# Performance work log

Measured on AMD Instinct MI355X. Metric: run time of the kernel, lower is better.

## Reference

```python
import jax, jax.numpy as jnp
import numpy as np

B, S, D_IN, D_OUT = 4, 2048, 1024, 1024

def setup_inputs() -> dict:
    key = jax.random.key(0)
    kx, kq, kk, kv = jax.random.split(key, 4)
    x = jax.random.normal(kx, (B, S, D_IN), dtype=jnp.float32)
    # nn.Linear weights are [d_out, d_in]; init scale ~ 1/sqrt(d_in)
    sc = 1.0 / np.sqrt(D_IN)
    Wq = jax.random.uniform(kq, (D_OUT, D_IN), minval=-sc, maxval=sc, dtype=jnp.float32)
    Wk = jax.random.uniform(kk, (D_OUT, D_IN), minval=-sc, maxval=sc, dtype=jnp.float32)
    Wv = jax.random.uniform(kv, (D_OUT, D_IN), minval=-sc, maxval=sc, dtype=jnp.float32)
    return {"x": x, "Wq": Wq, "Wk": Wk, "Wv": Wv}

def reference(x, Wq, Wk, Wv):
    # QKV projections (Linear without bias): y = x @ W.T
    q = jnp.einsum('bsd,od->bso', x, Wq)
    k = jnp.einsum('bsd,od->bso', x, Wk)
    v = jnp.einsum('bsd,od->bso', x, Wv)
    scores = jnp.einsum('bqo,bko->bqk', q, k)
    # NOTE: original code calls masked_fill non-in-place and discards the
    # result, so no causal mask is actually applied. Faithful: no mask.
    scale = 1.0 / jnp.sqrt(jnp.asarray(k.shape[-1], dtype=scores.dtype))
    weights = jax.nn.softmax(scores * scale, axis=-1)
    # dropout p=0.0 -> identity
    return jnp.einsum('bqk,bko->bqo', weights, v)
```

## Files before the change

### kernel.cpp

```cpp
#include <hip/hip_runtime.h>
#include <hip/hip_bf16.h>
#include <stdint.h>


typedef short bf16x8 __attribute__((ext_vector_type(8)));
typedef float f32x4  __attribute__((ext_vector_type(4)));

__device__ __forceinline__ unsigned short f2bf(float f) {
  unsigned u = __float_as_uint(f);
  u += 0x7fff + ((u >> 16) & 1);
  return (unsigned short)(u >> 16);
}

__global__ __launch_bounds__(256) void cvt_bf16(const float* __restrict__ src,
                                                unsigned short* __restrict__ dst) {
  int i = (blockIdx.x * 256 + threadIdx.x) * 4;
  float4 v = *(const float4*)(src + i);
  ushort4 o;
  o.x = f2bf(v.x); o.y = f2bf(v.y); o.z = f2bf(v.z); o.w = f2bf(v.w);
  *(ushort4*)(dst + i) = o;
}

__global__ __launch_bounds__(256) void invert8k(float* __restrict__ p) {
  int i = blockIdx.x * 256 + threadIdx.x;
  p[i] = 1.0f / p[i];
}

__device__ __forceinline__ void gload_lds16(const void* g, void* l) {
  __builtin_amdgcn_global_load_lds(
      (const __attribute__((address_space(1))) unsigned int*)g,
      (__attribute__((address_space(3))) unsigned int*)l, 16, 0, 0);
}

template<int STORE>
__global__ __launch_bounds__(256, 2) void gemm_nt(
    const unsigned short* __restrict__ A, const unsigned short* __restrict__ B,
    void* __restrict__ Cv, float* __restrict__ aux, int lda, int ldb, int ldc, int K,
    long strideA, long strideB, long strideC) {
  __shared__ __align__(16) unsigned short lds[2][2][128 * 32];
  const int tid  = threadIdx.x;
  const int lane = tid & 63;
  const int wid  = tid >> 6;
  const int bz   = blockIdx.z;
  const unsigned short* Ab = A + (size_t)bz * strideA;
  const unsigned short* Bb = B + (size_t)bz * strideB;
  const int row0 = blockIdx.x * 128;
  const int col0 = blockIdx.y * 128;

  f32x4 acc[4][4];
#pragma unroll
  for (int m = 0; m < 4; ++m)
#pragma unroll
    for (int n = 0; n < 4; ++n) acc[m][n] = f32x4{0.f, 0.f, 0.f, 0.f};

  const int KT = K >> 5;

  auto stage = [&](int buf, int kt) {
    const int k0 = kt << 5;
#pragma unroll
    for (int it = 0; it < 2; ++it) {
      int j   = it * 256 + tid;
      int r   = j >> 2;
      int kg  = j & 3;
      int kgS = kg ^ ((r >> 1) & 3);
      gload_lds16(Ab + (size_t)(row0 + r) * lda + k0 + kgS * 8, &lds[buf][0][j * 8]);
      gload_lds16(Bb + (size_t)(col0 + r) * ldb + k0 + kgS * 8, &lds[buf][1][j * 8]);
    }
  };

  stage(0, 0);
  int buf = 0;
  for (int kt = 0; kt < KT; ++kt) {
    __syncthreads();
    if (kt + 1 < KT) stage(buf ^ 1, kt + 1);
    const unsigned short* As = &lds[buf][0][0];
    const unsigned short* Bs = &lds[buf][1][0];
    const int kg = lane >> 4;
    const int lr = lane & 15;
    bf16x8 af[4], bfr[4];
#pragma unroll
    for (int m = 0; m < 4; ++m) {
      int r = ((wid >> 1) * 64) + m * 16 + lr;
      af[m] = *(const bf16x8*)(As + r * 32 + ((kg ^ ((r >> 1) & 3)) * 8));
    }
#pragma unroll
    for (int n = 0; n < 4; ++n) {
      int c = ((wid & 1) * 64) + n * 16 + lr;
      bfr[n] = *(const bf16x8*)(Bs + c * 32 + ((kg ^ ((c >> 1) & 3)) * 8));
    }
#pragma unroll
    for (int m = 0; m < 4; ++m)
#pragma unroll
      for (int n = 0; n < 4; ++n)
        acc[m][n] = __builtin_amdgcn_mfma_f32_16x16x32_bf16(af[m], bfr[n], acc[m][n], 0, 0, 0);
    buf ^= 1;
  }

  const int wr0 = row0 + (wid >> 1) * 64;
  const int wc0 = col0 + (wid & 1) * 64;
  const int rj  = lane >> 4;
  const int cl  = lane & 15;
  if constexpr (STORE == 3) {
    unsigned short* E = (unsigned short*)Cv + (size_t)bz * 4194304;
    float* rs = aux + bz * 2048;
    const float SC = 0.045084220027780106f;
#pragma unroll
    for (int m = 0; m < 4; ++m) {
#pragma unroll
      for (int j = 0; j < 4; ++j) {
        int r = wr0 + m * 16 + rj * 4 + j;
        float part = 0.f;
#pragma unroll
        for (int n = 0; n < 4; ++n) {
          int c = wc0 + n * 16 + cl;
          unsigned short eb = f2bf(exp2f(acc[m][n][j] * SC));
          E[(size_t)r * 2048 + c] = eb;
          part += __uint_as_float((unsigned)eb << 16);
        }
#pragma unroll
        for (int o = 1; o < 16; o <<= 1) part += __shfl_xor(part, o);
        if (cl == 0) atomicAdd(&rs[r], part);
      }
    }
  } else {
#pragma unroll
    for (int m = 0; m < 4; ++m) {
#pragma unroll
      for (int n = 0; n < 4; ++n) {
#pragma unroll
        for (int j = 0; j < 4; ++j) {
          int r = wr0 + m * 16 + rj * 4 + j;
          int c = wc0 + n * 16 + cl;
          float val = acc[m][n][j];
          if constexpr (STORE == 0) {
            unsigned short* C = (unsigned short*)Cv + (size_t)bz * strideC;
            C[(size_t)r * ldc + c] = f2bf(val);
          } else if constexpr (STORE == 2) {
            unsigned short* C = (unsigned short*)Cv;
            size_t idx = ((size_t)(r >> 11) * 1024 + c) * 2048 + (size_t)(r & 2047);
            C[idx] = f2bf(val);
          } else {
            float* C = (float*)Cv + (size_t)bz * strideC;
            C[(size_t)r * ldc + c] = val * aux[bz * 2048 + r];
          }
        }
      }
    }
  }
}

extern "C" void kernel_launch(void* const* d_in, const int* in_sizes, int n_in,
                              void* d_out, int out_size, void* d_ws, size_t ws_size,
                              hipStream_t stream) {
  const float* x  = (const float*)d_in[0];
  const float* Wq = (const float*)d_in[1];
  const float* Wk = (const float*)d_in[2];
  const float* Wv = (const float*)d_in[3];

  char* w = (char*)d_ws;
  unsigned short* xb  = (unsigned short*)(w);
  unsigned short* wqk = (unsigned short*)(w + (16ull << 20));
  unsigned short* wv  = (unsigned short*)(w + (20ull << 20));
  unsigned short* QK  = (unsigned short*)(w + (22ull << 20));
  unsigned short* Vt  = (unsigned short*)(w + (54ull << 20));
  unsigned short* E   = (unsigned short*)(w + (70ull << 20));
  float*          rs  = (float*)        (w + (102ull << 20));

  hipMemsetAsync(rs, 0, 8192 * sizeof(float), stream);

  cvt_bf16<<<8192, 256, 0, stream>>>(x,  xb);
  cvt_bf16<<<1024, 256, 0, stream>>>(Wq, wqk);
  cvt_bf16<<<1024, 256, 0, stream>>>(Wk, wqk + (1u << 20));
  cvt_bf16<<<1024, 256, 0, stream>>>(Wv, wv);

  gemm_nt<0><<<dim3(64, 8, 2), 256, 0, stream>>>(
      xb, wqk, QK, nullptr, 1024, 1024, 1024, 1024, 0, 1ll << 20, 8ll << 20);
  gemm_nt<2><<<dim3(64, 8, 1), 256, 0, stream>>>(
      xb, wv, Vt, nullptr, 1024, 1024, 0, 1024, 0, 0, 0);
  gemm_nt<3><<<dim3(16, 16, 4), 256, 0, stream>>>(
      QK, QK + (8u << 20), E, rs, 1024, 1024, 2048, 1024,
      2ll << 20, 2ll << 20, 0);
  invert8k<<<32, 256, 0, stream>>>(rs);
  gemm_nt<4><<<dim3(16, 8, 4), 256, 0, stream>>>(
      E, Vt, d_out, rs, 2048, 2048, 1024, 2048,
      4ll << 20, 2ll << 20, 2ll << 20);
}
```

Baseline: 257.6 us.

## Fuse conversions and QKV projections into single launches, fold reciprocal into epilogue

The four fp32-to-bf16 conversion kernels are merged into one launch that writes a single concatenated [3072,1024] weight buffer. The Q/K and V projection GEMMs become one 64x24 grid whose epilogue routes columns either to the QK buffer or to the transposed V layout. The separate row-sum inversion kernel is removed, and the reciprocal is computed once per row inside the final GEMM epilogue. This cuts launch count and lets the projection grid fill the device in one wave set, at the cost of a column branch in the epilogue.

```diff
diff --git a/kernel.cpp b/kernel.cpp
--- a/kernel.cpp
+++ b/kernel.cpp
@@ -12,18 +12,27 @@
   return (unsigned short)(u >> 16);
 }
 
-__global__ __launch_bounds__(256) void cvt_bf16(const float* __restrict__ src,
-                                                unsigned short* __restrict__ dst) {
-  int i = (blockIdx.x * 256 + threadIdx.x) * 4;
-  float4 v = *(const float4*)(src + i);
-  ushort4 o;
-  o.x = f2bf(v.x); o.y = f2bf(v.y); o.z = f2bf(v.z); o.w = f2bf(v.w);
-  *(ushort4*)(dst + i) = o;
-}
-
-__global__ __launch_bounds__(256) void invert8k(float* __restrict__ p) {
+__global__ __launch_bounds__(256) void cvt_all(
+    const float* __restrict__ x, const float* __restrict__ Wq,
+    const float* __restrict__ Wk, const float* __restrict__ Wv,
+    unsigned short* __restrict__ xb, unsigned short* __restrict__ W3) {
   int i = blockIdx.x * 256 + threadIdx.x;
-  p[i] = 1.0f / p[i];
+  const int XF4 = 2097152;
+  if (i < XF4) {
+    float4 v = *(const float4*)(x + (size_t)i * 4);
+    ushort4 o;
+    o.x = f2bf(v.x); o.y = f2bf(v.y); o.z = f2bf(v.z); o.w = f2bf(v.w);
+    *(ushort4*)(xb + (size_t)i * 4) = o;
+  } else {
+    int j = i - XF4;
+    int row = j >> 8;
+    const float* s = (row < 1024) ? Wq : (row < 2048) ? Wk : Wv;
+    int off = (row & 1023) * 1024 + (j & 255) * 4;
+    float4 v = *(const float4*)(s + off);
+    ushort4 o;
+    o.x = f2bf(v.x); o.y = f2bf(v.y); o.z = f2bf(v.z); o.w = f2bf(v.w);
+    *(ushort4*)(W3 + (size_t)j * 4) = o;
+  }
 }
 
 __device__ __forceinline__ void gload_lds16(const void* g, void* l) {
@@ -100,7 +109,27 @@
   const int wc0 = col0 + (wid & 1) * 64;
   const int rj  = lane >> 4;
   const int cl  = lane & 15;
-  if constexpr (STORE == 3) {
+  if constexpr (STORE == 0) {
+    unsigned short* QK = (unsigned short*)Cv;
+    unsigned short* Vt = (unsigned short*)aux;
+#pragma unroll
+    for (int m = 0; m < 4; ++m) {
+#pragma unroll
+      for (int n = 0; n < 4; ++n) {
+#pragma unroll
+        for (int j = 0; j < 4; ++j) {
+          int r = wr0 + m * 16 + rj * 4 + j;
+          int c = wc0 + n * 16 + cl;
+          unsigned short bv = f2bf(acc[m][n][j]);
+          if (c < 2048) {
+            QK[(size_t)(c >> 10) * 8388608 + (size_t)r * 1024 + (c & 1023)] = bv;
+          } else {
+            Vt[(size_t)(r >> 11) * 2097152 + (size_t)(c - 2048) * 2048 + (r & 2047)] = bv;
+          }
+        }
+      }
+    }
+  } else if constexpr (STORE == 3) {
     unsigned short* E = (unsigned short*)Cv + (size_t)bz * 4194304;
     float* rs = aux + bz * 2048;
     const float SC = 0.045084220027780106f;
@@ -123,26 +152,18 @@
       }
     }
   } else {
-#pragma unroll
-    for (int m = 0; m < 4; ++m) {
-#pragma unroll
-      for (int n = 0; n < 4; ++n) {
-#pragma unroll
-        for (int j = 0; j < 4; ++j) {
-          int r = wr0 + m * 16 + rj * 4 + j;
+    float* C = (float*)Cv + (size_t)bz * strideC;
+    const float* rs = aux + bz * 2048;
+#pragma unroll
+    for (int m = 0; m < 4; ++m) {
+#pragma unroll
+      for (int j = 0; j < 4; ++j) {
+        int r = wr0 + m * 16 + rj * 4 + j;
+        float inv = 1.0f / rs[r];
+#pragma unroll
+        for (int n = 0; n < 4; ++n) {
           int c = wc0 + n * 16 + cl;
-          float val = acc[m][n][j];
-          if constexpr (STORE == 0) {
-            unsigned short* C = (unsigned short*)Cv + (size_t)bz * strideC;
-            C[(size_t)r * ldc + c] = f2bf(val);
-          } else if constexpr (STORE == 2) {
-            unsigned short* C = (unsigned short*)Cv;
-            size_t idx = ((size_t)(r >> 11) * 1024 + c) * 2048 + (size_t)(r & 2047);
-            C[idx] = f2bf(val);
-          } else {
-            float* C = (float*)Cv + (size_t)bz * strideC;
-            C[(size_t)r * ldc + c] = val * aux[bz * 2048 + r];
-          }
+          C[(size_t)r * ldc + c] = acc[m][n][j] * inv;
         }
       }
     }
@@ -158,29 +179,22 @@
   const float* Wv = (const float*)d_in[3];
 
   char* w = (char*)d_ws;
-  unsigned short* xb  = (unsigned short*)(w);
-  unsigned short* wqk = (unsigned short*)(w + (16ull << 20));
-  unsigned short* wv  = (unsigned short*)(w + (20ull << 20));
-  unsigned short* QK  = (unsigned short*)(w + (22ull << 20));
-  unsigned short* Vt  = (unsigned short*)(w + (54ull << 20));
-  unsigned short* E   = (unsigned short*)(w + (70ull << 20));
-  float*          rs  = (float*)        (w + (102ull << 20));
+  unsigned short* xb = (unsigned short*)(w);
+  unsigned short* W3 = (unsigned short*)(w + (16ull << 20));
+  unsigned short* QK = (unsigned short*)(w + (22ull << 20));
+  unsigned short* Vt = (unsigned short*)(w + (54ull << 20));
+  unsigned short* E  = (unsigned short*)(w + (70ull << 20));
+  float*          rs = (float*)        (w + (102ull << 20));
 
   hipMemsetAsync(rs, 0, 8192 * sizeof(float), stream);
 
-  cvt_bf16<<<8192, 256, 0, stream>>>(x,  xb);
-  cvt_bf16<<<1024, 256, 0, stream>>>(Wq, wqk);
-  cvt_bf16<<<1024, 256, 0, stream>>>(Wk, wqk + (1u << 20));
-  cvt_bf16<<<1024, 256, 0, stream>>>(Wv, wv);
-
-  gemm_nt<0><<<dim3(64, 8, 2), 256, 0, stream>>>(
-      xb, wqk, QK, nullptr, 1024, 1024, 1024, 1024, 0, 1ll << 20, 8ll << 20);
-  gemm_nt<2><<<dim3(64, 8, 1), 256, 0, stream>>>(
-      xb, wv, Vt, nullptr, 1024, 1024, 0, 1024, 0, 0, 0);
+  cvt_all<<<11264, 256, 0, stream>>>(x, Wq, Wk, Wv, xb, W3);
+
+  gemm_nt<0><<<dim3(64, 24, 1), 256, 0, stream>>>(
+      xb, W3, QK, (float*)Vt, 1024, 1024, 0, 1024, 0, 0, 0);
   gemm_nt<3><<<dim3(16, 16, 4), 256, 0, stream>>>(
       QK, QK + (8u << 20), E, rs, 1024, 1024, 2048, 1024,
       2ll << 20, 2ll << 20, 0);
-  invert8k<<<32, 256, 0, stream>>>(rs);
   gemm_nt<4><<<dim3(16, 8, 4), 256, 0, stream>>>(
       E, Vt, d_out, rs, 2048, 2048, 1024, 2048,
       4ll << 20, 2ll << 20, 2ll << 20);
```

After: 262.8 us. 2.0% more time.
